# Kernel optimization log

Hardware: AMD Instinct MI355X
Metric: run time of the kernel (lower is better)

The kernel has to match this reference:

```python
import jax, jax.numpy as jnp
import numpy as np

N = 4096
D = 256
TEMP = 0.1
NEG_INF = -1e30
NUM_IDS = 1000
NUM_CAMS = 8


def setup_inputs() -> dict:
    key = jax.random.key(0)
    k1, k2, k3 = jax.random.split(key, 3)
    features = jax.random.normal(k1, (N, 2, D), dtype=jnp.float32)
    label = jax.random.randint(k2, (N,), 0, NUM_IDS)
    camid = jax.random.randint(k3, (N,), 0, NUM_CAMS)
    return {"features": features, "label": label, "camid": camid}


def reference(features, label, camid):
    n = features.shape[0]
    n2 = 2 * n
    # torch.cat(torch.unbind(features, dim=1), dim=0): [N,2,D] -> [2N,D]
    f = jnp.concatenate([features[:, 0], features[:, 1]], axis=0)
    # pairwise similarity, pre-scaled by 1/temperature (original divides each
    # per-positive logit row by T, which is equivalent)
    logit = jnp.matmul(f, f.T) / TEMP  # [2N, 2N]
    diag = jnp.eye(n2, dtype=bool)
    lg = jnp.where(diag, NEG_INF, logit)  # diagonal excluded by masked_select
    m = jnp.max(lg, axis=1, keepdims=True)  # stable shift per row
    e = jnp.exp(lg - m)  # exp(logit - m), 0 on diagonal

    label_eq = label[:, None] == label[None, :]          # [N, N]
    cam_eq = camid[:, None] == camid[None, :]
    pos_id = jnp.tile(label_eq, (2, 2))                  # label_mask.repeat(2,2)
    pos_cam = jnp.tile(label_eq & cam_eq, (2, 2))        # is_pos.repeat(2,2)

    def branch(pos_full, row_scale):
        pm = pos_full & ~diag        # positives (off-diagonal)
        nm = ~pos_full               # negatives (diagonal is positive -> excluded)
        neg_sum = jnp.sum(jnp.where(nm, e, 0.0), axis=1, keepdims=True)
        # per-positive CE with label 0 over [positive, negatives]:
        #   log(exp(l_p - m) + neg_sum) + m - l_p
        per = jnp.log(jnp.where(pm, e + neg_sum, 1.0)) - (lg - m)
        num_pos = jnp.sum(pm, axis=1).astype(lg.dtype)
        row = jnp.sum(jnp.where(pm, per, 0.0), axis=1) / num_pos
        return row_scale * row

    loss_rows = branch(pos_id, 1.0) + branch(pos_cam, 0.5)
    loss = jnp.sum(loss_rows) / n2
    return loss
```

## Files before the change

kernel.cpp:

```cpp
#include <hip/hip_runtime.h>

typedef __attribute__((ext_vector_type(8))) _Float16 h8v;
typedef __attribute__((ext_vector_type(8))) short    s8v;
typedef __attribute__((ext_vector_type(4))) float    f4v;

#define N_   4096
#define N2   8192
#define D_   256
#define NIDS 1000
#define LCAP 32

constexpr float INV_TEMP = 10.0f;
constexpr float K_LOG2   = 14.426950408889634f;
constexpr float LN2F     = 0.6931471805599453f;
constexpr float NEGINF   = -1e30f;

__device__ __forceinline__ const float* frow(const float* f, int r) {
    return f + (size_t)(r & (N_ - 1)) * (2 * D_) + (size_t)((r >> 12) * D_);
}

__device__ __forceinline__ void gload_lds16(const void* g, void* l) {
    __builtin_amdgcn_global_load_lds(
        (const __attribute__((address_space(1))) void*)g,
        (__attribute__((address_space(3))) void*)l, 16, 0, 0);
}

__global__ __launch_bounds__(256) void prepK(const float* __restrict__ feat,
                                             const int* __restrict__ label,
                                             _Float16* __restrict__ f16,
                                             int* __restrict__ lists,
                                             int* __restrict__ done) {
    if (blockIdx.x < 1024) {
        int t = blockIdx.x * 256 + threadIdx.x;
        int r = t >> 5, g = t & 31;
        const float* src = frow(feat, r) + g * 8;
        float4 v0 = *(const float4*)src;
        float4 v1 = *(const float4*)(src + 4);
        float x[8] = {v0.x, v0.y, v0.z, v0.w, v1.x, v1.y, v1.z, v1.w};
        h8v h;
        #pragma unroll
        for (int i = 0; i < 8; ++i) h[i] = (_Float16)x[i];
        *(h8v*)(f16 + (size_t)r * D_ + g * 8) = h;
    } else {
        if (blockIdx.x == 1024 && threadIdx.x == 0) *done = 0;
        int cls  = (blockIdx.x - 1024) * 4 + (threadIdx.x >> 6);
        int lane = threadIdx.x & 63;
        int* Lp = lists + (size_t)cls * (LCAP + 1);
        int cnt = 0;
        for (int jj = 0; jj < N_; jj += 64) {
            unsigned long long mk = __ballot(label[jj + lane] == cls);
            while (mk) {
                int b = __ffsll((unsigned long long)mk) - 1;
                mk &= mk - 1;
                if (lane == 0 && cnt < LCAP) Lp[1 + cnt] = jj + b;
                ++cnt;
            }
        }
        if (lane == 0) Lp[0] = (cnt < LCAP) ? cnt : LCAP;
    }
}

__global__ __launch_bounds__(256, 4) void phaseA(const _Float16* __restrict__ f16,
                                                 const int* __restrict__ label,
                                                 float2* __restrict__ partial) {
    __shared__ char lds[32768];

    const int tid  = threadIdx.x;
    const int lane = tid & 63;
    const int w    = tid >> 6;
    const int wr   = w >> 1, wc = w & 1;

    int idx = (blockIdx.x & 7) * 260 + (blockIdx.x >> 3);
    int rt = 0, rem = idx;
    while (rem >= 64 - rt) { rem -= 64 - rt; ++rt; }
    const int ct = rt + rem;
    const bool offdiag = (ct != rt);
    const int rowBase = rt * 128, colBase = ct * 128;

    f4v acc[4][4];
    #pragma unroll
    for (int i = 0; i < 4; ++i)
        #pragma unroll
        for (int j = 0; j < 4; ++j) acc[i][j] = (f4v){0.f, 0.f, 0.f, 0.f};

    const int prB = (w < 2) ? rowBase : colBase;
    const int ssrc = (lane & 3) ^ ((lane >> 3) & 3);
    const _Float16* gl = f16 + (size_t)(prB + (w & 1) * 64 + (lane >> 2)) * D_ + ssrc * 8;
    const int ldoff = ((w >= 2) ? 8192 : 0) + (w & 1) * 4096 + lane * 16;

    #pragma unroll
    for (int i = 0; i < 4; ++i)
        gload_lds16(gl + (size_t)i * 16 * D_, lds + ldoff + i * 1024);
    __syncthreads();

    const int l15  = lane & 15;
    const int phys = ((lane >> 4) ^ ((l15 >> 1) & 3)) * 16;
    const int aoff0 = (wr * 64 + l15) * 64 + phys;
    const int boff0 = 8192 + (wc * 64 + l15) * 64 + phys;

    for (int kc = 0; kc < 8; ++kc) {
        const int cur = kc & 1;
        if (kc < 7) {
            const _Float16* gk = gl + (kc + 1) * 32;
            char* lp = lds + (cur ^ 1) * 16384 + ldoff;
            #pragma unroll
            for (int i = 0; i < 4; ++i)
                gload_lds16(gk + (size_t)i * 16 * D_, lp + i * 1024);
        }
        const char* bb = lds + cur * 16384;
        h8v a[4], b[4];
        #pragma unroll
        for (int rf = 0; rf < 4; ++rf) a[rf] = *(const h8v*)(bb + aoff0 + rf * 1024);
        #pragma unroll
        for (int cf = 0; cf < 4; ++cf) b[cf] = *(const h8v*)(bb + boff0 + cf * 1024);
        #pragma unroll
        for (int rf = 0; rf < 4; ++rf)
            #pragma unroll
            for (int cf = 0; cf < 4; ++cf)
                acc[rf][cf] = __builtin_amdgcn_mfma_f32_16x16x32_f16(a[rf], b[cf], acc[rf][cf], 0, 0, 0);
        __syncthreads();
    }

    float* rowm  = (float*)lds;
    float* colm  = (float*)(lds + 16896);
    float* mrowS = (float*)(lds + 21504);
    float* mcolS = (float*)(lds + 22016);

    const int grp32 = wc * 16 + l15;
    const int grp8  = wr * 4 + (lane >> 4);
    int rloc[16], cloc[4];
    int rowlab[16], collab[4];
    #pragma unroll
    for (int rf = 0; rf < 4; ++rf)
        #pragma unroll
        for (int rg = 0; rg < 4; ++rg) {
            int i = rf * 4 + rg;
            rloc[i] = wr * 64 + rf * 16 + (lane >> 4) * 4 + rg;
            rowlab[i] = label[(rowBase + rloc[i]) & (N_ - 1)];
        }
    #pragma unroll
    for (int cf = 0; cf < 4; ++cf) {
        cloc[cf] = wc * 64 + cf * 16 + l15;
        collab[cf] = label[(colBase + cloc[cf]) & (N_ - 1)];
    }

    #pragma unroll
    for (int rf = 0; rf < 4; ++rf)
        #pragma unroll
        for (int cf = 0; cf < 4; ++cf)
            #pragma unroll
            for (int rg = 0; rg < 4; ++rg) {
                float v = acc[rf][cf][rg] * K_LOG2;
                acc[rf][cf][rg] = (collab[cf] == rowlab[rf * 4 + rg]) ? NEGINF : v;
            }

    #pragma unroll
    for (int rf = 0; rf < 4; ++rf)
        #pragma unroll
        for (int rg = 0; rg < 4; ++rg) {
            float m = fmaxf(fmaxf(acc[rf][0][rg], acc[rf][1][rg]),
                            fmaxf(acc[rf][2][rg], acc[rf][3][rg]));
            rowm[rloc[rf * 4 + rg] * 33 + grp32] = m;
        }
    if (offdiag) {
        #pragma unroll
        for (int cf = 0; cf < 4; ++cf) {
            float m = NEGINF;
            #pragma unroll
            for (int rf = 0; rf < 4; ++rf)
                #pragma unroll
                for (int rg = 0; rg < 4; ++rg) m = fmaxf(m, acc[rf][cf][rg]);
            colm[cloc[cf] * 9 + grp8] = m;
        }
    }
    __syncthreads();
    if (tid < 128) {
        float m = NEGINF;
        #pragma unroll
        for (int g = 0; g < 32; ++g) m = fmaxf(m, rowm[tid * 33 + g]);
        mrowS[tid] = m;
        if (offdiag) {
            float mc = NEGINF;
            #pragma unroll
            for (int g = 0; g < 8; ++g) mc = fmaxf(mc, colm[tid * 9 + g]);
            mcolS[tid] = mc;
        }
    }
    __syncthreads();

    #pragma unroll
    for (int rf = 0; rf < 4; ++rf)
        #pragma unroll
        for (int rg = 0; rg < 4; ++rg) {
            int i = rf * 4 + rg;
            float m = mrowS[rloc[i]];
            float s = 0.f;
            #pragma unroll
            for (int cf = 0; cf < 4; ++cf) s += exp2f(acc[rf][cf][rg] - m);
            rowm[rloc[i] * 33 + grp32] = s;
        }
    if (offdiag) {
        #pragma unroll
        for (int cf = 0; cf < 4; ++cf) {
            float m = mcolS[cloc[cf]];
            float s = 0.f;
            #pragma unroll
            for (int rf = 0; rf < 4; ++rf)
                #pragma unroll
                for (int rg = 0; rg < 4; ++rg) s += exp2f(acc[rf][cf][rg] - m);
            colm[cloc[cf] * 9 + grp8] = s;
        }
    }
    __syncthreads();
    if (tid < 128) {
        float s = 0.f;
        #pragma unroll
        for (int g = 0; g < 32; ++g) s += rowm[tid * 33 + g];
        partial[(size_t)(rowBase + tid) * 64 + ct] = make_float2(mrowS[tid], s);
        if (offdiag) {
            float s2 = 0.f;
            #pragma unroll
            for (int g = 0; g < 8; ++g) s2 += colm[tid * 9 + g];
            partial[(size_t)(colBase + tid) * 64 + rt] = make_float2(mcolS[tid], s2);
        }
    }
}

__global__ __launch_bounds__(512) void phaseB(const float* __restrict__ feat,
                                              const int* __restrict__ label,
                                              const int* __restrict__ camid,
                                              const int* __restrict__ lists,
                                              const float2* __restrict__ partial,
                                              float* __restrict__ rowloss,
                                              int* __restrict__ done,
                                              float* __restrict__ out) {
    __shared__ int   cList[8][64];
    __shared__ int   fList[8][64];
    __shared__ float pList[8][64];
    __shared__ float red[512];
    __shared__ int   lastFlag;

    const int tid = threadIdx.x, lane = tid & 63, w = tid >> 6;
    const int row = blockIdx.x * 8 + w;
    const int rl = label[row & (N_ - 1)];
    const int rc = camid[row & (N_ - 1)];

    float2 p = partial[(size_t)row * 64 + lane];
    float mm = p.x, ms = p.y;
    #pragma unroll
    for (int off = 32; off >= 1; off >>= 1) {
        float om = __shfl_xor(mm, off), os = __shfl_xor(ms, off);
        float nm = fmaxf(mm, om);
        ms = ms * exp2f(mm - nm) + os * exp2f(om - nm);
        mm = nm;
    }
    const float cid = (mm + __log2f(ms)) * LN2F;

    const int li = lane & 15, g = lane >> 4;
    const float4* fip = (const float4*)frow(feat, row);
    float4 fiv[4];
    #pragma unroll
    for (int k = 0; k < 4; ++k) fiv[k] = fip[li * 4 + k];

    const int* Lp = lists + (size_t)rl * (LCAP + 1);
    const int nmem = Lp[0];
    int jm = (lane < 2 * nmem) ? Lp[1 + (lane >> 1)] : -1;
    int cand = jm + (lane & 1) * N_;
    bool valid = (jm >= 0) && (cand != row);
    unsigned long long mask = __ballot(valid);
    int cnt = __popcll(mask);
    int pos = __popcll(mask & ((1ull << lane) - 1ull));
    if (valid) {
        cList[w][pos] = cand;
        fList[w][pos] = (camid[jm] == rc) ? 1 : 0;
    }

    const int nb = (cnt + 3) >> 2;
    for (int b = 0; b < nb; ++b) {
        int e = b * 4 + g;
        bool act = (e < cnt);
        int c = act ? cList[w][e] : row;
        const float4* fcp = (const float4*)frow(feat, c);
        float pp = 0.f;
        #pragma unroll
        for (int k = 0; k < 4; ++k) {
            float4 v = fcp[li * 4 + k];
            pp += fiv[k].x * v.x + fiv[k].y * v.y + fiv[k].z * v.z + fiv[k].w * v.w;
        }
        #pragma unroll
        for (int off = 8; off >= 1; off >>= 1) pp += __shfl_xor(pp, off);
        if (act && li == 0) pList[w][e] = pp * INV_TEMP;
    }

    float a_e = (lane < cnt) ? pList[w][lane] : NEGINF;
    int   f_e = (lane < cnt) ? fList[w][lane] : 1;

    float xa = (f_e == 0) ? a_e : NEGINF;
    float mx = xa;
    #pragma unroll
    for (int off = 32; off >= 1; off >>= 1) mx = fmaxf(mx, __shfl_xor(mx, off));
    float xe = (f_e == 0) ? __expf(xa - mx) : 0.f;
    #pragma unroll
    for (int off = 32; off >= 1; off >>= 1) xe += __shfl_xor(xe, off);
    float ccam;
    if (xe > 0.f) {
        float xl = mx + __logf(xe);
        float d = xl - cid;
        ccam = (d <= 0.f) ? cid + log1pf(__expf(d)) : xl + log1pf(__expf(-d));
    } else {
        ccam = cid;
    }

    float ti = cid - a_e;
    float termid = (ti <= 0.f) ? log1pf(__expf(ti)) : ti + log1pf(__expf(-ti));
    termid = (lane < cnt) ? termid : 0.f;
    float tc = ccam - a_e;
    float termcam = (tc <= 0.f) ? log1pf(__expf(tc)) : tc + log1pf(__expf(-tc));
    termcam = (lane < cnt && f_e) ? termcam : 0.f;
    #pragma unroll
    for (int off = 32; off >= 1; off >>= 1) {
        termid  += __shfl_xor(termid, off);
        termcam += __shfl_xor(termcam, off);
    }
    int ncam = __popcll(__ballot(lane < cnt && f_e));
    if (lane == 0)
        rowloss[row] = termid / (float)cnt + 0.5f * termcam / (float)ncam;

    __syncthreads();
    if (tid == 0) {
        __threadfence();
        lastFlag = (atomicAdd(done, 1) == (int)gridDim.x - 1) ? 1 : 0;
    }
    __syncthreads();
    if (lastFlag) {
        __threadfence();
        float s = 0.f;
        const int b0 = tid * 16;
        #pragma unroll
        for (int i = 0; i < 16; ++i) s += rowloss[b0 + i];
        red[tid] = s;
        __syncthreads();
        for (int ww = 256; ww > 0; ww >>= 1) {
            if (tid < ww) red[tid] += red[tid + ww];
            __syncthreads();
        }
        if (tid == 0) out[0] = red[0] / (float)N2;
    }
}

extern "C" void kernel_launch(void* const* d_in, const int* in_sizes, int n_in,
                              void* d_out, int out_size, void* d_ws, size_t ws_size,
                              hipStream_t stream) {
    const float* feat  = (const float*)d_in[0];
    const int*   label = (const int*)d_in[1];
    const int*   camid = (const int*)d_in[2];

    _Float16* f16    = (_Float16*)d_ws;
    float2*   partial = (float2*)((char*)d_ws + 4u * 1024 * 1024);
    float*    rowloss = (float*)((char*)d_ws + 8u * 1024 * 1024);
    int*      lists   = (int*)(rowloss + N2);
    int*      done    = lists + NIDS * (LCAP + 1);

    prepK<<<1274, 256, 0, stream>>>(feat, label, f16, lists, done);
    phaseA<<<2080, 256, 0, stream>>>(f16, label, partial);
    phaseB<<<1024, 512, 0, stream>>>(feat, label, camid, lists, partial,
                                     rowloss, done, (float*)d_out);
}
```

Measured before the change: 95.60 us.

## Fuse fp16 conversion and label-list build into the GEMM kernel

Removes the separate prep kernel: phaseA now reads fp32 features directly, converts them to fp16 in registers and writes them into LDS, with register-staged prefetch interleaved between MFMA groups. The per-class label-list construction and the done-flag reset move into the first 250 blocks of phaseA. This saves a kernel launch and the fp16 workspace round trip. In exchange it doubles global read bytes per tile, drops the async global-to-LDS loads in favour of VGPR staging, and puts extra serial work on some GEMM blocks.

```diff
diff --git a/kernel.cpp b/kernel.cpp
--- a/kernel.cpp
+++ b/kernel.cpp
@@ -1,7 +1,6 @@
 #include <hip/hip_runtime.h>
 
 typedef __attribute__((ext_vector_type(8))) _Float16 h8v;
-typedef __attribute__((ext_vector_type(8))) short    s8v;
 typedef __attribute__((ext_vector_type(4))) float    f4v;
 
 #define N_   4096
@@ -19,32 +18,30 @@
     return f + (size_t)(r & (N_ - 1)) * (2 * D_) + (size_t)((r >> 12) * D_);
 }
 
-__device__ __forceinline__ void gload_lds16(const void* g, void* l) {
-    __builtin_amdgcn_global_load_lds(
-        (const __attribute__((address_space(1))) void*)g,
-        (__attribute__((address_space(3))) void*)l, 16, 0, 0);
+__device__ __forceinline__ void wr16(void* p, float4 x, float4 y) {
+    h8v h;
+    h[0] = (_Float16)x.x; h[1] = (_Float16)x.y; h[2] = (_Float16)x.z; h[3] = (_Float16)x.w;
+    h[4] = (_Float16)y.x; h[5] = (_Float16)y.y; h[6] = (_Float16)y.z; h[7] = (_Float16)y.w;
+    *(h8v*)p = h;
 }
 
-__global__ __launch_bounds__(256) void prepK(const float* __restrict__ feat,
-                                             const int* __restrict__ label,
-                                             _Float16* __restrict__ f16,
-                                             int* __restrict__ lists,
-                                             int* __restrict__ done) {
-    if (blockIdx.x < 1024) {
-        int t = blockIdx.x * 256 + threadIdx.x;
-        int r = t >> 5, g = t & 31;
-        const float* src = frow(feat, r) + g * 8;
-        float4 v0 = *(const float4*)src;
-        float4 v1 = *(const float4*)(src + 4);
-        float x[8] = {v0.x, v0.y, v0.z, v0.w, v1.x, v1.y, v1.z, v1.w};
-        h8v h;
-        #pragma unroll
-        for (int i = 0; i < 8; ++i) h[i] = (_Float16)x[i];
-        *(h8v*)(f16 + (size_t)r * D_ + g * 8) = h;
-    } else {
-        if (blockIdx.x == 1024 && threadIdx.x == 0) *done = 0;
-        int cls  = (blockIdx.x - 1024) * 4 + (threadIdx.x >> 6);
-        int lane = threadIdx.x & 63;
+__global__ __launch_bounds__(256, 4) void phaseA(const float* __restrict__ feat,
+                                                 const int* __restrict__ label,
+                                                 float2* __restrict__ partial,
+                                                 int* __restrict__ lists,
+                                                 int* __restrict__ done) {
+    __shared__ char lds[32768];
+
+    const int tid  = threadIdx.x;
+    const int lane = tid & 63;
+    const int w    = tid >> 6;
+    const int wr   = w >> 1, wc = w & 1;
+    const int l15  = lane & 15;
+
+    if (blockIdx.x == 0 && tid == 0) *done = 0;
+
+    if (blockIdx.x < 250) {
+        int cls = blockIdx.x * 4 + w;
         int* Lp = lists + (size_t)cls * (LCAP + 1);
         int cnt = 0;
         for (int jj = 0; jj < N_; jj += 64) {
@@ -58,17 +55,6 @@
         }
         if (lane == 0) Lp[0] = (cnt < LCAP) ? cnt : LCAP;
     }
-}
-
-__global__ __launch_bounds__(256, 4) void phaseA(const _Float16* __restrict__ f16,
-                                                 const int* __restrict__ label,
-                                                 float2* __restrict__ partial) {
-    __shared__ char lds[32768];
-
-    const int tid  = threadIdx.x;
-    const int lane = tid & 63;
-    const int w    = tid >> 6;
-    const int wr   = w >> 1, wc = w & 1;
 
     int idx = (blockIdx.x & 7) * 260 + (blockIdx.x >> 3);
     int rt = 0, rem = idx;
@@ -83,43 +69,91 @@
         #pragma unroll
         for (int j = 0; j < 4; ++j) acc[i][j] = (f4v){0.f, 0.f, 0.f, 0.f};
 
-    const int prB = (w < 2) ? rowBase : colBase;
+    const int prB  = (w < 2) ? rowBase : colBase;
     const int ssrc = (lane & 3) ^ ((lane >> 3) & 3);
-    const _Float16* gl = f16 + (size_t)(prB + (w & 1) * 64 + (lane >> 2)) * D_ + ssrc * 8;
+    const int r0   = prB + (w & 1) * 64 + (lane >> 2);
+    const float* rp[4];
+    #pragma unroll
+    for (int i = 0; i < 4; ++i) rp[i] = frow(feat, r0 + 16 * i) + ssrc * 8;
     const int ldoff = ((w >= 2) ? 8192 : 0) + (w & 1) * 4096 + lane * 16;
 
-    #pragma unroll
-    for (int i = 0; i < 4; ++i)
-        gload_lds16(gl + (size_t)i * 16 * D_, lds + ldoff + i * 1024);
-    __syncthreads();
-
-    const int l15  = lane & 15;
-    const int phys = ((lane >> 4) ^ ((l15 >> 1) & 3)) * 16;
+    {
+        float4 t0 = *(const float4*)(rp[0]),     t1 = *(const float4*)(rp[0] + 4);
+        float4 t2 = *(const float4*)(rp[1]),     t3 = *(const float4*)(rp[1] + 4);
+        wr16(lds + ldoff,        t0, t1);
+        wr16(lds + ldoff + 1024, t2, t3);
+        t0 = *(const float4*)(rp[2]);  t1 = *(const float4*)(rp[2] + 4);
+        t2 = *(const float4*)(rp[3]);  t3 = *(const float4*)(rp[3] + 4);
+        wr16(lds + ldoff + 2048, t0, t1);
+        wr16(lds + ldoff + 3072, t2, t3);
+    }
+
+    const int phys  = ((lane >> 4) ^ ((l15 >> 1) & 3)) * 16;
     const int aoff0 = (wr * 64 + l15) * 64 + phys;
     const int boff0 = 8192 + (wc * 64 + l15) * 64 + phys;
 
     for (int kc = 0; kc < 8; ++kc) {
         const int cur = kc & 1;
-        if (kc < 7) {
-            const _Float16* gk = gl + (kc + 1) * 32;
-            char* lp = lds + (cur ^ 1) * 16384 + ldoff;
-            #pragma unroll
-            for (int i = 0; i < 4; ++i)
-                gload_lds16(gk + (size_t)i * 16 * D_, lp + i * 1024);
-        }
+        __syncthreads();
         const char* bb = lds + cur * 16384;
-        h8v a[4], b[4];
-        #pragma unroll
-        for (int rf = 0; rf < 4; ++rf) a[rf] = *(const h8v*)(bb + aoff0 + rf * 1024);
-        #pragma unroll
-        for (int cf = 0; cf < 4; ++cf) b[cf] = *(const h8v*)(bb + boff0 + cf * 1024);
-        #pragma unroll
-        for (int rf = 0; rf < 4; ++rf)
-            #pragma unroll
-            for (int cf = 0; cf < 4; ++cf)
-                acc[rf][cf] = __builtin_amdgcn_mfma_f32_16x16x32_f16(a[rf], b[cf], acc[rf][cf], 0, 0, 0);
-        __syncthreads();
-    }
+        char* wp = lds + (cur ^ 1) * 16384 + ldoff;
+        const bool st = (kc < 7);
+        const int kB = (kc + 1) * 32;
+
+        float4 t0, t1, t2, t3;
+        if (st) {
+            t0 = *(const float4*)(rp[0] + kB); t1 = *(const float4*)(rp[0] + kB + 4);
+            t2 = *(const float4*)(rp[1] + kB); t3 = *(const float4*)(rp[1] + kB + 4);
+        }
+
+        h8v a0 = *(const h8v*)(bb + aoff0);
+        h8v a1 = *(const h8v*)(bb + aoff0 + 1024);
+        h8v a2 = *(const h8v*)(bb + aoff0 + 2048);
+        h8v a3 = *(const h8v*)(bb + aoff0 + 3072);
+
+        {
+            h8v b = *(const h8v*)(bb + boff0);
+            acc[0][0] = __builtin_amdgcn_mfma_f32_16x16x32_f16(a0, b, acc[0][0], 0, 0, 0);
+            acc[1][0] = __builtin_amdgcn_mfma_f32_16x16x32_f16(a1, b, acc[1][0], 0, 0, 0);
+            acc[2][0] = __builtin_amdgcn_mfma_f32_16x16x32_f16(a2, b, acc[2][0], 0, 0, 0);
+            acc[3][0] = __builtin_amdgcn_mfma_f32_16x16x32_f16(a3, b, acc[3][0], 0, 0, 0);
+        }
+        {
+            h8v b = *(const h8v*)(bb + boff0 + 1024);
+            acc[0][1] = __builtin_amdgcn_mfma_f32_16x16x32_f16(a0, b, acc[0][1], 0, 0, 0);
+            acc[1][1] = __builtin_amdgcn_mfma_f32_16x16x32_f16(a1, b, acc[1][1], 0, 0, 0);
+            acc[2][1] = __builtin_amdgcn_mfma_f32_16x16x32_f16(a2, b, acc[2][1], 0, 0, 0);
+            acc[3][1] = __builtin_amdgcn_mfma_f32_16x16x32_f16(a3, b, acc[3][1], 0, 0, 0);
+        }
+
+        if (st) {
+            wr16(wp,        t0, t1);
+            wr16(wp + 1024, t2, t3);
+            t0 = *(const float4*)(rp[2] + kB); t1 = *(const float4*)(rp[2] + kB + 4);
+            t2 = *(const float4*)(rp[3] + kB); t3 = *(const float4*)(rp[3] + kB + 4);
+        }
+
+        {
+            h8v b = *(const h8v*)(bb + boff0 + 2048);
+            acc[0][2] = __builtin_amdgcn_mfma_f32_16x16x32_f16(a0, b, acc[0][2], 0, 0, 0);
+            acc[1][2] = __builtin_amdgcn_mfma_f32_16x16x32_f16(a1, b, acc[1][2], 0, 0, 0);
+            acc[2][2] = __builtin_amdgcn_mfma_f32_16x16x32_f16(a2, b, acc[2][2], 0, 0, 0);
+            acc[3][2] = __builtin_amdgcn_mfma_f32_16x16x32_f16(a3, b, acc[3][2], 0, 0, 0);
+        }
+        {
+            h8v b = *(const h8v*)(bb + boff0 + 3072);
+            acc[0][3] = __builtin_amdgcn_mfma_f32_16x16x32_f16(a0, b, acc[0][3], 0, 0, 0);
+            acc[1][3] = __builtin_amdgcn_mfma_f32_16x16x32_f16(a1, b, acc[1][3], 0, 0, 0);
+            acc[2][3] = __builtin_amdgcn_mfma_f32_16x16x32_f16(a2, b, acc[2][3], 0, 0, 0);
+            acc[3][3] = __builtin_amdgcn_mfma_f32_16x16x32_f16(a3, b, acc[3][3], 0, 0, 0);
+        }
+
+        if (st) {
+            wr16(wp + 2048, t0, t1);
+            wr16(wp + 3072, t2, t3);
+        }
+    }
+    __syncthreads();
 
     float* rowm  = (float*)lds;
     float* colm  = (float*)(lds + 16896);
@@ -355,14 +389,12 @@
     const int*   label = (const int*)d_in[1];
     const int*   camid = (const int*)d_in[2];
 
-    _Float16* f16    = (_Float16*)d_ws;
-    float2*   partial = (float2*)((char*)d_ws + 4u * 1024 * 1024);
-    float*    rowloss = (float*)((char*)d_ws + 8u * 1024 * 1024);
-    int*      lists   = (int*)(rowloss + N2);
-    int*      done    = lists + NIDS * (LCAP + 1);
-
-    prepK<<<1274, 256, 0, stream>>>(feat, label, f16, lists, done);
-    phaseA<<<2080, 256, 0, stream>>>(f16, label, partial);
+    float2* partial = (float2*)d_ws;
+    float*  rowloss = (float*)((char*)d_ws + 4u * 1024 * 1024);
+    int*    lists   = (int*)(rowloss + N2);
+    int*    done    = lists + NIDS * (LCAP + 1);
+
+    phaseA<<<2080, 256, 0, stream>>>(feat, label, partial, lists, done);
     phaseB<<<1024, 512, 0, stream>>>(feat, label, camid, lists, partial,
                                      rowloss, done, (float*)d_out);
 }
```

New measurement: 93.21 us (median of 3 runs). 1.03x faster.
